# Performance work log

Hardware: AMD Instinct MI355X
Metric: run time of the kernel (lower is better)

## Reference

```python
import jax, jax.numpy as jnp
import numpy as np

B, C, H, W_IMG = 16, 3, 384, 384
P = 16
G = H // P                 # 24
NPATCH = G * G             # 576
SEQ = NPATCH + 1           # 577 (with cls token)
D, FF, NH, NL = 768, 3072, 12, 12
NCLS = 1000
K = int(0.5 * NPATCH)
HD = D // NH
EPS = 1e-6


def _ln(x, g, b):
    mu = jnp.mean(x, axis=-1, keepdims=True)
    var = jnp.mean((x - mu) ** 2, axis=-1, keepdims=True)
    return (x - mu) * jax.lax.rsqrt(var + EPS) * g + b


def setup_inputs() -> dict:
    key = jax.random.key(0)
    ks = jax.random.split(key, 12)
    s = 0.02
    return {
        "x": jax.random.normal(ks[0], (B, C, H, W_IMG), jnp.float32),
        "patch_w": jax.random.normal(ks[1], (D, C, P, P), jnp.float32) * s,
        "patch_b": jnp.zeros((D,), jnp.float32),
        "cls_tok": jax.random.normal(ks[2], (1, 1, D), jnp.float32) * s,
        "pos_emb": jax.random.normal(ks[3], (1, SEQ, D), jnp.float32) * s,
        "ln1_g": jnp.ones((NL, D), jnp.float32),
        "ln1_b": jnp.zeros((NL, D), jnp.float32),
        "Wqkv": jax.random.normal(ks[4], (NL, D, 3 * D), jnp.float32) * s,
        "bqkv": jnp.zeros((NL, 3 * D), jnp.float32),
        "Wo": jax.random.normal(ks[5], (NL, D, D), jnp.float32) * s,
        "bo": jnp.zeros((NL, D), jnp.float32),
        "ln2_g": jnp.ones((NL, D), jnp.float32),
        "ln2_b": jnp.zeros((NL, D), jnp.float32),
        "W1": jax.random.normal(ks[6], (NL, D, FF), jnp.float32) * s,
        "b1": jnp.zeros((NL, FF), jnp.float32),
        "W2": jax.random.normal(ks[7], (NL, FF, D), jnp.float32) * s,
        "b2": jnp.zeros((NL, D), jnp.float32),
        "lnf_g": jnp.ones((D,), jnp.float32),
        "lnf_b": jnp.zeros((D,), jnp.float32),
        "fc_w": jax.random.normal(ks[8], (D, NCLS), jnp.float32) * s,
        "fc_b": jnp.zeros((NCLS,), jnp.float32),
    }


def reference(x, patch_w, patch_b, cls_tok, pos_emb, ln1_g, ln1_b, Wqkv, bqkv,
              Wo, bo, ln2_g, ln2_b, W1, b1, W2, b2, lnf_g, lnf_b, fc_w, fc_b):
    b = x.shape[0]
    # patch embedding: strided conv -> (b, D, G, G) -> (b, NPATCH, D)
    patches = jax.lax.conv_general_dilated(
        x, patch_w, window_strides=(P, P), padding="VALID",
        dimension_numbers=("NCHW", "OIHW", "NCHW")) + patch_b[None, :, None, None]
    tok = patches.reshape(b, D, NPATCH).transpose(0, 2, 1)
    tok = jnp.concatenate([jnp.broadcast_to(cls_tok, (b, 1, D)), tok], axis=1)
    tok = tok + pos_emb  # seq matches original_seq_len, no resize

    # saliency = avg-pool of raw first input channel (net_G output is unused in the source)
    pooled = x[:, 0].reshape(b, G, P, G, P).mean(axis=(2, 4)).reshape(b, NPATCH)
    _, idx = jax.lax.top_k(jnp.abs(pooled), K)          # (b, K)
    spatial = tok[:, 1:, :]
    sel = jnp.take_along_axis(spatial, idx[:, :, None], axis=1)  # (b, K, D)
    h = jnp.concatenate([tok[:, :1, :], sel], axis=1)   # (b, K+1, D)
    S = h.shape[1]

    scale = 1.0 / np.sqrt(HD)
    for i in range(NL):
        y = _ln(h, ln1_g[i], ln1_b[i])
        qkv = y @ Wqkv[i] + bqkv[i]
        q, k_, v = jnp.split(qkv, 3, axis=-1)
        q = q.reshape(b, S, NH, HD)
        k_ = k_.reshape(b, S, NH, HD)
        v = v.reshape(b, S, NH, HD)
        att = jnp.einsum("bqhd,bkhd->bhqk", q, k_) * scale
        att = jax.nn.softmax(att, axis=-1)
        o = jnp.einsum("bhqk,bkhd->bqhd", att, v).reshape(b, S, D)
        h = h + (o @ Wo[i] + bo[i])
        y = _ln(h, ln2_g[i], ln2_b[i])
        h = h + (jax.nn.gelu(y @ W1[i] + b1[i], approximate=False) @ W2[i] + b2[i])

    cls_out = _ln(h, lnf_g, lnf_b)[:, 0]   # pool_type='tok'
    return cls_out @ fc_w + fc_b


if __name__ == "__main__":
    out = reference(**setup_inputs())
    print(out.shape)
```

## Files before the change

kernel.cpp:

```cpp
#include <hip/hip_runtime.h>
#include <hip/hip_bf16.h>
#include <math.h>

#define BB 16
#define SS 289
#define DD 768
#define FFD 3072
#define NHD 12
#define NLAY 12
#define KSEL 288
#define NPATCH 576

typedef short bf16x8 __attribute__((ext_vector_type(8)));
typedef short bf16x4 __attribute__((ext_vector_type(4)));
typedef float f32x4 __attribute__((ext_vector_type(4)));

typedef __attribute__((address_space(3))) void lds_t;
typedef __attribute__((address_space(1))) const void glb_t;

__device__ __forceinline__ void gload16(const void* g, void* l) {
    __builtin_amdgcn_global_load_lds((glb_t*)g, (lds_t*)l, 16, 0, 0);
}

__device__ __forceinline__ bf16x8 ds_read128(unsigned addr) {
    bf16x8 r;
    asm volatile("ds_read_b128 %0, %1" : "=v"(r) : "v"(addr));
    return r;
}

__device__ __forceinline__ float gelu_f(float v) {
    return 0.5f * v * (1.0f + erff(v * 0.70710678118654752f));
}

__device__ __forceinline__ void store_val(float* p, float v) { *p = v; }
__device__ __forceinline__ void store_val(__hip_bfloat16* p, float v) { *p = __float2bfloat16(v); }

__global__ __launch_bounds__(256) void pool_kernel(const float* __restrict__ x,
                                                   float* __restrict__ pooled) {
    int bp = blockIdx.x;
    int b = bp / NPATCH, p = bp - b * NPATCH;
    int gi = p / 24, gj = p - gi * 24;
    int tid = threadIdx.x;
    int pi = tid >> 4, pj = tid & 15;
    float v = x[((size_t)(b * 3) * 384 + gi * 16 + pi) * 384 + gj * 16 + pj];
    #pragma unroll
    for (int o = 32; o > 0; o >>= 1) v += __shfl_down(v, o);
    __shared__ float red[4];
    if ((tid & 63) == 0) red[tid >> 6] = v;
    __syncthreads();
    if (tid == 0) pooled[bp] = (red[0] + red[1] + red[2] + red[3]) * (1.0f / 256.0f);
}

__global__ __launch_bounds__(576) void topk_kernel(const float* __restrict__ pooled,
                                                   int* __restrict__ idxsel) {
    __shared__ float a[NPATCH];
    int b = blockIdx.x, tid = threadIdx.x;
    a[tid] = fabsf(pooled[b * NPATCH + tid]);
    __syncthreads();
    float mine = a[tid];
    int rank = 0;
    for (int j = 0; j < NPATCH; ++j) {
        float aj = a[j];
        rank += (aj > mine) || (aj == mine && j < tid);
    }
    if (rank < KSEL) idxsel[b * KSEL + rank] = tid;
}

__global__ __launch_bounds__(256) void convert_bf16(const float* __restrict__ in,
                                                    __hip_bfloat16* __restrict__ out,
                                                    int n) {
    int i = blockIdx.x * 256 + threadIdx.x;
    if (i < n) out[i] = __float2bfloat16(in[i]);
}

__global__ __launch_bounds__(256) void convert_layer(const float* __restrict__ wqkv,
                                                     const float* __restrict__ wo,
                                                     const float* __restrict__ w1,
                                                     const float* __restrict__ w2,
                                                     __hip_bfloat16* __restrict__ oqkv,
                                                     __hip_bfloat16* __restrict__ owo,
                                                     __hip_bfloat16* __restrict__ ow1,
                                                     __hip_bfloat16* __restrict__ ow2) {
    __shared__ float tb[32][33];
    int bid = blockIdx.x;
    const float* W; __hip_bfloat16* O; int K, N, tile;
    if (bid < 1728)      { W = wqkv; O = oqkv; K = 768;  N = 2304; tile = bid; }
    else if (bid < 2304) { W = wo;   O = owo;  K = 768;  N = 768;  tile = bid - 1728; }
    else if (bid < 4608) { W = w1;   O = ow1;  K = 768;  N = 3072; tile = bid - 2304; }
    else                 { W = w2;   O = ow2;  K = 3072; N = 768;  tile = bid - 4608; }
    int ntx = N >> 5;
    int n0 = (tile % ntx) << 5, k0 = (tile / ntx) << 5;
    int t = threadIdx.x;
    int r = t >> 3, c = (t & 7) << 2;
    float4 v = *(const float4*)&W[(size_t)(k0 + r) * N + n0 + c];
    tb[r][c] = v.x; tb[r][c + 1] = v.y; tb[r][c + 2] = v.z; tb[r][c + 3] = v.w;
    __syncthreads();
    int n = t >> 3, k = (t & 7) << 2;
    __hip_bfloat16* dst = &O[(size_t)(n0 + n) * K + k0 + k];
    #pragma unroll
    for (int j = 0; j < 4; ++j) dst[j] = __float2bfloat16(tb[k + j][n]);
}

__global__ __launch_bounds__(256) void im2col_kernel(const float* __restrict__ x,
                                                     const int* __restrict__ idxsel,
                                                     __hip_bfloat16* __restrict__ col) {
    int t = blockIdx.x;
    int b = t / KSEL, r = t - b * KSEL;
    int p = idxsel[b * KSEL + r];
    int gi = p / 24, gj = p - gi * 24;
    int tid = threadIdx.x;
    int pi = tid >> 4, pj = tid & 15;
    __hip_bfloat16* crow = col + (size_t)t * 768;
    #pragma unroll
    for (int c = 0; c < 3; ++c)
        crow[c * 256 + tid] = __float2bfloat16(
            x[((size_t)(b * 3 + c) * 384 + gi * 16 + pi) * 384 + gj * 16 + pj]);
}

__global__ __launch_bounds__(256) void assemble_tokens(const float* __restrict__ temp,
                                                       const float* __restrict__ cls_tok,
                                                       const float* __restrict__ pos_emb,
                                                       const int* __restrict__ idxsel,
                                                       float* __restrict__ h) {
    int row = blockIdx.x;
    int b = row / SS, s = row - b * SS;
    int tid = threadIdx.x;
    float* hrow = h + (size_t)row * DD;
    if (s == 0) {
        #pragma unroll
        for (int c = 0; c < 3; ++c) {
            int j = c * 256 + tid;
            hrow[j] = cls_tok[j] + pos_emb[j];
        }
    } else {
        int r = s - 1;
        int p = idxsel[b * KSEL + r];
        const float* trow = temp + (size_t)(b * KSEL + r) * DD;
        const float* pe = pos_emb + (size_t)(1 + p) * DD;
        #pragma unroll
        for (int c = 0; c < 3; ++c) {
            int j = c * 256 + tid;
            hrow[j] = trow[j] + pe[j];
        }
    }
}

template <typename T>
__global__ __launch_bounds__(256) void ln_kernel(const float* __restrict__ in,
                                                 T* __restrict__ out,
                                                 const float* __restrict__ g,
                                                 const float* __restrict__ be,
                                                 size_t in_stride) {
    int row = blockIdx.x;
    const float* r = in + (size_t)row * in_stride;
    T* w = out + (size_t)row * DD;
    int tid = threadIdx.x;
    float v0 = r[tid], v1 = r[256 + tid], v2 = r[512 + tid];
    float s = v0 + v1 + v2;
    #pragma unroll
    for (int o = 32; o > 0; o >>= 1) s += __shfl_down(s, o);
    __shared__ float red[4];
    if ((tid & 63) == 0) red[tid >> 6] = s;
    __syncthreads();
    float mu = (red[0] + red[1] + red[2] + red[3]) * (1.0f / 768.0f);
    float d0 = v0 - mu, d1 = v1 - mu, d2 = v2 - mu;
    float q = d0 * d0 + d1 * d1 + d2 * d2;
    #pragma unroll
    for (int o = 32; o > 0; o >>= 1) q += __shfl_down(q, o);
    __syncthreads();
    if ((tid & 63) == 0) red[tid >> 6] = q;
    __syncthreads();
    float var = (red[0] + red[1] + red[2] + red[3]) * (1.0f / 768.0f);
    float rs = rsqrtf(var + 1e-6f);
    store_val(&w[tid],       d0 * rs * g[tid]       + be[tid]);
    store_val(&w[256 + tid], d1 * rs * g[256 + tid] + be[256 + tid]);
    store_val(&w[512 + tid], d2 * rs * g[512 + tid] + be[512 + tid]);
}

template <typename OUT_T, int ACT, int RES, int SPLITK>
__global__ __launch_bounds__(512) void gemm_bf16(const __hip_bfloat16* __restrict__ A,
                                                 const __hip_bfloat16* __restrict__ BT,
                                                 OUT_T* __restrict__ C,
                                                 const float* __restrict__ bias,
                                                 const float* __restrict__ res,
                                                 float* __restrict__ part,
                                                 int M, int N, int K) {
    __shared__ __hip_bfloat16 smA[3][256 * 32];
    __shared__ __hip_bfloat16 smB[3][256 * 32];
    const int t = threadIdx.x;
    const int lane = t & 63, wid = t >> 6;
    const int wr = wid >> 2, wc = wid & 3;
    const int l15 = lane & 15, l4 = lane >> 4;

    const int gx = gridDim.x;
    const int nwg = gx * gridDim.y;
    const int orig = blockIdx.y * gx + blockIdx.x;
    const int q8 = nwg >> 3, r8 = nwg & 7;
    const int xcd = orig & 7, linb = orig >> 3;
    const int swz = (xcd < r8 ? xcd * (q8 + 1) : r8 * (q8 + 1) + (xcd - r8) * q8) + linb;
    const int m0 = (swz / gx) << 8;
    const int n0 = (swz - (swz / gx) * gx) << 8;

    const int Ksub = K / SPLITK;
    const int kz0 = blockIdx.z * Ksub;

    int ra[8], rb[4];
    #pragma unroll
    for (int f = 0; f < 8; ++f) {
        int ml = wr * 128 + f * 16 + l15;
        ra[f] = ml * 64 + ((l4 ^ ((ml >> 1) & 3)) << 4);
    }
    #pragma unroll
    for (int f = 0; f < 4; ++f) {
        int nl = wc * 64 + f * 16 + l15;
        rb[f] = nl * 64 + ((l4 ^ ((nl >> 1) & 3)) << 4);
    }

    size_t aoff[2], boff[2];
    #pragma unroll
    for (int it = 0; it < 2; ++it) {
        int s = it * 512 + t;
        int m = s >> 2;
        int kc = (s & 3) ^ ((m >> 1) & 3);
        int gm = m0 + m; if (gm > M - 1) gm = M - 1;
        aoff[it] = (size_t)gm * K + kz0 + kc * 8;
        boff[it] = (size_t)(n0 + m) * K + kz0 + kc * 8;
    }
    const int wb = wid << 10;
    const unsigned ldsA0 = (unsigned)(size_t)(lds_t*)&smA[0][0];
    const unsigned ldsB0 = (unsigned)(size_t)(lds_t*)&smB[0][0];

    auto STAGE = [&](int kt, int buf) {
        int k0e = kt << 5;
        gload16(A + aoff[0] + k0e,  (char*)(&smA[buf][0]) + wb);
        gload16(A + aoff[1] + k0e,  (char*)(&smA[buf][0]) + 8192 + wb);
        gload16(BT + boff[0] + k0e, (char*)(&smB[buf][0]) + wb);
        gload16(BT + boff[1] + k0e, (char*)(&smB[buf][0]) + 8192 + wb);
    };

    f32x4 acc[8][4];
    #pragma unroll
    for (int i = 0; i < 8; ++i)
        #pragma unroll
        for (int j = 0; j < 4; ++j) acc[i][j] = (f32x4){0.f, 0.f, 0.f, 0.f};

    const int nt = Ksub >> 5;
    STAGE(0, 0); STAGE(1, 1);
    int cur = 0, stb = 2;
    for (int kt = 0; kt < nt; ++kt) {
        if (kt + 1 < nt) asm volatile("s_waitcnt vmcnt(4)" ::: "memory");
        else             asm volatile("s_waitcnt vmcnt(0)" ::: "memory");
        asm volatile("s_barrier" ::: "memory");
        if (kt + 2 < nt) STAGE(kt + 2, stb);
        const unsigned sa = ldsA0 + cur * 16384u;
        const unsigned sb = ldsB0 + cur * 16384u;
        bf16x8 af[8], bf[4];
        #pragma unroll
        for (int f = 0; f < 8; ++f) af[f] = ds_read128(sa + ra[f]);
        #pragma unroll
        for (int f = 0; f < 4; ++f) bf[f] = ds_read128(sb + rb[f]);
        asm volatile("s_waitcnt lgkmcnt(0)" ::: "memory");
        __builtin_amdgcn_sched_barrier(0);
        #pragma unroll
        for (int i = 0; i < 8; ++i)
            #pragma unroll
            for (int j = 0; j < 4; ++j)
                acc[i][j] = __builtin_amdgcn_mfma_f32_16x16x32_bf16(af[i], bf[j], acc[i][j], 0, 0, 0);
        cur = cur == 2 ? 0 : cur + 1;
        stb = stb == 2 ? 0 : stb + 1;
    }

    if (SPLITK == 1) {
        #pragma unroll
        for (int i = 0; i < 8; ++i) {
            int gmb = m0 + wr * 128 + i * 16 + l4 * 4;
            #pragma unroll
            for (int j = 0; j < 4; ++j) {
                int gn = n0 + wc * 64 + j * 16 + l15;
                float bv = bias ? bias[gn] : 0.f;
                #pragma unroll
                for (int r = 0; r < 4; ++r) {
                    int gm = gmb + r;
                    if (gm < M) {
                        float v = acc[i][j][r] + bv;
                        if (ACT) v = gelu_f(v);
                        if (RES) v += res[(size_t)gm * N + gn];
                        store_val(&C[(size_t)gm * N + gn], v);
                    }
                }
            }
        }
    } else {
        float* pz = part + (size_t)blockIdx.z * M * N;
        #pragma unroll
        for (int i = 0; i < 8; ++i) {
            int gmb = m0 + wr * 128 + i * 16 + l4 * 4;
            #pragma unroll
            for (int j = 0; j < 4; ++j) {
                int gn = n0 + wc * 64 + j * 16 + l15;
                #pragma unroll
                for (int r = 0; r < 4; ++r) {
                    int gm = gmb + r;
                    if (gm < M) pz[(size_t)gm * N + gn] = acc[i][j][r];
                }
            }
        }
    }
}

template <int NPART>
__global__ __launch_bounds__(256) void combine_res(const float* __restrict__ part,
                                                   const float* __restrict__ bias,
                                                   float* __restrict__ h,
                                                   int MN, int N) {
    int i = (blockIdx.x * 256 + threadIdx.x) * 4;
    if (i >= MN) return;
    float4 v = *(const float4*)&part[i];
    #pragma unroll
    for (int z = 1; z < NPART; ++z) {
        float4 p = *(const float4*)&part[(size_t)z * MN + i];
        v.x += p.x; v.y += p.y; v.z += p.z; v.w += p.w;
    }
    int n = i % N;
    float4 bv = *(const float4*)&bias[n];
    float4 hv = *(const float4*)&h[i];
    v.x += bv.x + hv.x; v.y += bv.y + hv.y; v.z += bv.z + hv.z; v.w += bv.w + hv.w;
    *(float4*)&h[i] = v;
}

__global__ __launch_bounds__(256) void head_gemm(const float* __restrict__ yf,
                                                 const float* __restrict__ fc_w,
                                                 const float* __restrict__ fc_b,
                                                 float* __restrict__ out) {
    __shared__ float ylds[4 * 768];
    const int tid = threadIdx.x;
    const int mh = blockIdx.y * 4;
    for (int i = tid; i < 4 * 768; i += 256) ylds[i] = yf[(size_t)(mh + i / 768) * 768 + i % 768];
    __syncthreads();
    const int n = blockIdx.x * 256 + tid;
    if (n >= 1000) return;
    float acc0 = 0.f, acc1 = 0.f, acc2 = 0.f, acc3 = 0.f;
    for (int k = 0; k < 768; ++k) {
        float w = fc_w[(size_t)k * 1000 + n];
        acc0 = fmaf(ylds[k], w, acc0);
        acc1 = fmaf(ylds[768 + k], w, acc1);
        acc2 = fmaf(ylds[1536 + k], w, acc2);
        acc3 = fmaf(ylds[2304 + k], w, acc3);
    }
    float b = fc_b[n];
    out[(size_t)(mh + 0) * 1000 + n] = acc0 + b;
    out[(size_t)(mh + 1) * 1000 + n] = acc1 + b;
    out[(size_t)(mh + 2) * 1000 + n] = acc2 + b;
    out[(size_t)(mh + 3) * 1000 + n] = acc3 + b;
}

__global__ __launch_bounds__(64) void attn_fused(const __hip_bfloat16* __restrict__ qkv,
                                                 __hip_bfloat16* __restrict__ o) {
    __shared__ __hip_bfloat16 p_lds[32][40];
    __shared__ __hip_bfloat16 v_lds[32][68];
    const int qt = blockIdx.x, bh = blockIdx.y;
    const int b = bh / NHD, hd = bh - b * NHD;
    const int lane = threadIdx.x;
    const int l15 = lane & 15, l4 = lane >> 4;
    const size_t tb = (size_t)b * SS;
    const int hc = hd * 64;

    bf16x8 aq[2][2];
    #pragma unroll
    for (int qi = 0; qi < 2; ++qi) {
        int qr = qt * 32 + qi * 16 + l15;
        if (qr >= SS) qr = SS - 1;
        const __hip_bfloat16* qrow = qkv + (tb + qr) * 2304 + hc;
        #pragma unroll
        for (int kd = 0; kd < 2; ++kd)
            aq[qi][kd] = *(const bf16x8*)(qrow + kd * 32 + l4 * 8);
    }

    float m_run[2][4], l_run[2][4];
    f32x4 oa[2][4];
    #pragma unroll
    for (int qi = 0; qi < 2; ++qi)
        #pragma unroll
        for (int r = 0; r < 4; ++r) { m_run[qi][r] = -1e30f; l_run[qi][r] = 0.f; }
    #pragma unroll
    for (int qi = 0; qi < 2; ++qi)
        #pragma unroll
        for (int dt = 0; dt < 4; ++dt) oa[qi][dt] = (f32x4){0.f, 0.f, 0.f, 0.f};

    for (int kt = 0; kt < 10; ++kt) {
        const int kbase = kt * 32;
        bf16x4 vreg[8];
        #pragma unroll
        for (int it = 0; it < 8; ++it) {
            int vr = kbase + it * 4 + l4;
            if (vr >= SS) vr = SS - 1;
            vreg[it] = *(const bf16x4*)(qkv + (tb + vr) * 2304 + 1536 + hc + l15 * 4);
        }
        bf16x8 bk[2][2];
        #pragma unroll
        for (int ki = 0; ki < 2; ++ki) {
            int kr = kbase + ki * 16 + l15;
            if (kr >= SS) kr = SS - 1;
            const __hip_bfloat16* krow = qkv + (tb + kr) * 2304 + 768 + hc;
            #pragma unroll
            for (int kd = 0; kd < 2; ++kd)
                bk[ki][kd] = *(const bf16x8*)(krow + kd * 32 + l4 * 8);
        }
        f32x4 s[2][2];
        #pragma unroll
        for (int qi = 0; qi < 2; ++qi)
            #pragma unroll
            for (int ki = 0; ki < 2; ++ki) {
                f32x4 a = (f32x4){0.f, 0.f, 0.f, 0.f};
                #pragma unroll
                for (int kd = 0; kd < 2; ++kd)
                    a = __builtin_amdgcn_mfma_f32_16x16x32_bf16(aq[qi][kd], bk[ki][kd], a, 0, 0, 0);
                s[qi][ki] = a;
            }
        #pragma unroll
        for (int ki = 0; ki < 2; ++ki) {
            bool valid = (kbase + ki * 16 + l15) < SS;
            #pragma unroll
            for (int qi = 0; qi < 2; ++qi)
                #pragma unroll
                for (int r = 0; r < 4; ++r)
                    s[qi][ki][r] = valid ? s[qi][ki][r] * 0.125f : -1e30f;
        }
        float p[2][2][4];
        #pragma unroll
        for (int qi = 0; qi < 2; ++qi) {
            float tm[4];
            #pragma unroll
            for (int r = 0; r < 4; ++r) tm[r] = fmaxf(s[qi][0][r], s[qi][1][r]);
            #pragma unroll
            for (int sh = 1; sh < 16; sh <<= 1)
                #pragma unroll
                for (int r = 0; r < 4; ++r) tm[r] = fmaxf(tm[r], __shfl_xor(tm[r], sh));
            float rs[4];
            #pragma unroll
            for (int r = 0; r < 4; ++r) {
                float mn = fmaxf(m_run[qi][r], tm[r]);
                float corr = __expf(m_run[qi][r] - mn);
                m_run[qi][r] = mn;
                float p0 = __expf(s[qi][0][r] - mn);
                float p1 = __expf(s[qi][1][r] - mn);
                p[qi][0][r] = p0; p[qi][1][r] = p1;
                rs[r] = p0 + p1;
                l_run[qi][r] *= corr;
                #pragma unroll
                for (int dt = 0; dt < 4; ++dt) oa[qi][dt][r] *= corr;
            }
            #pragma unroll
            for (int sh = 1; sh < 16; sh <<= 1)
                #pragma unroll
                for (int r = 0; r < 4; ++r) rs[r] += __shfl_xor(rs[r], sh);
            #pragma unroll
            for (int r = 0; r < 4; ++r) l_run[qi][r] += rs[r];
        }
        #pragma unroll
        for (int qi = 0; qi < 2; ++qi)
            #pragma unroll
            for (int ki = 0; ki < 2; ++ki)
                #pragma unroll
                for (int r = 0; r < 4; ++r)
                    p_lds[qi * 16 + l4 * 4 + r][ki * 16 + l15] = __float2bfloat16(p[qi][ki][r]);
        #pragma unroll
        for (int it = 0; it < 8; ++it)
            *(bf16x4*)&v_lds[it * 4 + l4][l15 * 4] = vreg[it];
        __syncthreads();
        bf16x8 pa[2];
        #pragma unroll
        for (int qi = 0; qi < 2; ++qi)
            pa[qi] = *(const bf16x8*)&p_lds[qi * 16 + l15][l4 * 8];
        bf16x8 vb[4];
        #pragma unroll
        for (int dt = 0; dt < 4; ++dt) {
            bf16x8 v;
            #pragma unroll
            for (int j = 0; j < 8; ++j)
                v[j] = *(const short*)&v_lds[l4 * 8 + j][dt * 16 + l15];
            vb[dt] = v;
        }
        #pragma unroll
        for (int qi = 0; qi < 2; ++qi)
            #pragma unroll
            for (int dt = 0; dt < 4; ++dt)
                oa[qi][dt] = __builtin_amdgcn_mfma_f32_16x16x32_bf16(pa[qi], vb[dt], oa[qi][dt], 0, 0, 0);
        __syncthreads();
    }
    #pragma unroll
    for (int qi = 0; qi < 2; ++qi)
        #pragma unroll
        for (int r = 0; r < 4; ++r) {
            int q = qt * 32 + qi * 16 + l4 * 4 + r;
            if (q < SS) {
                float inv = 1.0f / l_run[qi][r];
                __hip_bfloat16* orow = o + (tb + q) * 768 + hc;
                #pragma unroll
                for (int dt = 0; dt < 4; ++dt)
                    orow[dt * 16 + l15] = __float2bfloat16(oa[qi][dt][r] * inv);
            }
        }
}

static const size_t OFF_POOLED = 0;
static const size_t OFF_IDX    = 10240;
static const size_t OFF_H      = 16384;
static const size_t OFF_YB     = 3567616;
static const size_t OFF_OB     = 5343232;
static const size_t OFF_QKVB   = 7118848;
static const size_t OFF_WBUF   = 12445696;
static const size_t OFF_PWB    = 15984640;
static const size_t OFF_YF     = 16279552;
static const size_t OFF_BIG    = 16291840;
static const size_t OFF_PART   = 23394304;

extern "C" void kernel_launch(void* const* d_in, const int* in_sizes, int n_in,
                              void* d_out, int out_size, void* d_ws, size_t ws_size,
                              hipStream_t stream) {
    const float* x       = (const float*)d_in[0];
    const float* patch_w = (const float*)d_in[1];
    const float* patch_b = (const float*)d_in[2];
    const float* cls_tok = (const float*)d_in[3];
    const float* pos_emb = (const float*)d_in[4];
    const float* ln1_g   = (const float*)d_in[5];
    const float* ln1_b   = (const float*)d_in[6];
    const float* Wqkv    = (const float*)d_in[7];
    const float* bqkv    = (const float*)d_in[8];
    const float* Wo      = (const float*)d_in[9];
    const float* bo      = (const float*)d_in[10];
    const float* ln2_g   = (const float*)d_in[11];
    const float* ln2_b   = (const float*)d_in[12];
    const float* W1      = (const float*)d_in[13];
    const float* b1      = (const float*)d_in[14];
    const float* W2      = (const float*)d_in[15];
    const float* b2      = (const float*)d_in[16];
    const float* lnf_g   = (const float*)d_in[17];
    const float* lnf_b   = (const float*)d_in[18];
    const float* fc_w    = (const float*)d_in[19];
    const float* fc_b    = (const float*)d_in[20];
    float* out = (float*)d_out;
    float* ws  = (float*)d_ws;

    float*          pooled = ws + OFF_POOLED;
    int*            idxsel = (int*)(ws + OFF_IDX);
    float*          h      = ws + OFF_H;
    __hip_bfloat16* yb     = (__hip_bfloat16*)(ws + OFF_YB);
    __hip_bfloat16* ob     = (__hip_bfloat16*)(ws + OFF_OB);
    __hip_bfloat16* qkvb   = (__hip_bfloat16*)(ws + OFF_QKVB);
    __hip_bfloat16* wbuf   = (__hip_bfloat16*)(ws + OFF_WBUF);
    __hip_bfloat16* pwb    = (__hip_bfloat16*)(ws + OFF_PWB);
    float*          yf     = ws + OFF_YF;
    float*          big    = ws + OFF_BIG;
    float*          part   = ws + OFF_PART;
    __hip_bfloat16* col    = (__hip_bfloat16*)big;
    float*          temp   = big + 1769472;
    __hip_bfloat16* hidden = (__hip_bfloat16*)big;

    __hip_bfloat16* wqkvT = wbuf;
    __hip_bfloat16* woT   = wbuf + 1769472;
    __hip_bfloat16* w1T   = wbuf + 2359296;
    __hip_bfloat16* w2T   = wbuf + 4718592;

    const int M = BB * SS;
    const int MG2 = 19;
    const int MN = M * DD;

    pool_kernel<<<BB * NPATCH, 256, 0, stream>>>(x, pooled);
    topk_kernel<<<BB, 576, 0, stream>>>(pooled, idxsel);
    convert_bf16<<<(589824 + 255) / 256, 256, 0, stream>>>(patch_w, pwb, 589824);
    im2col_kernel<<<BB * KSEL, 256, 0, stream>>>(x, idxsel, col);
    gemm_bf16<float, 0, 0, 1><<<dim3(3, 18), 512, 0, stream>>>(
        col, pwb, temp, patch_b, nullptr, nullptr, 4608, DD, DD);
    assemble_tokens<<<BB * SS, 256, 0, stream>>>(temp, cls_tok, pos_emb, idxsel, h);

    for (int i = 0; i < NLAY; ++i) {
        convert_layer<<<6912, 256, 0, stream>>>(Wqkv + (size_t)i * DD * 3 * DD,
                                                Wo + (size_t)i * DD * DD,
                                                W1 + (size_t)i * DD * FFD,
                                                W2 + (size_t)i * FFD * DD,
                                                wqkvT, woT, w1T, w2T);

        ln_kernel<__hip_bfloat16><<<M, 256, 0, stream>>>(h, yb, ln1_g + i * DD, ln1_b + i * DD, DD);
        gemm_bf16<__hip_bfloat16, 0, 0, 1><<<dim3(9, MG2), 512, 0, stream>>>(
            yb, wqkvT, qkvb, bqkv + (size_t)i * 3 * DD, nullptr, nullptr, M, 3 * DD, DD);
        attn_fused<<<dim3(10, BB * NHD), 64, 0, stream>>>(qkvb, ob);
        gemm_bf16<float, 0, 0, 2><<<dim3(3, MG2, 2), 512, 0, stream>>>(
            ob, woT, (float*)nullptr, nullptr, nullptr, part, M, DD, DD);
        combine_res<2><<<(MN / 4 + 255) / 256, 256, 0, stream>>>(part, bo + (size_t)i * DD, h, MN, DD);
        ln_kernel<__hip_bfloat16><<<M, 256, 0, stream>>>(h, yb, ln2_g + i * DD, ln2_b + i * DD, DD);
        gemm_bf16<__hip_bfloat16, 1, 0, 1><<<dim3(12, MG2), 512, 0, stream>>>(
            yb, w1T, hidden, b1 + (size_t)i * FFD, nullptr, nullptr, M, FFD, DD);
        gemm_bf16<float, 0, 0, 4><<<dim3(3, MG2, 4), 512, 0, stream>>>(
            hidden, w2T, (float*)nullptr, nullptr, nullptr, part, M, DD, FFD);
        combine_res<4><<<(MN / 4 + 255) / 256, 256, 0, stream>>>(part, b2 + (size_t)i * DD, h, MN, DD);
    }

    ln_kernel<float><<<BB, 256, 0, stream>>>(h, yf, lnf_g, lnf_b, (size_t)SS * DD);
    head_gemm<<<dim3(4, 4), 256, 0, stream>>>(yf, fc_w, fc_b, out);
}
```

Measured before the change: 2.799 ms.

## Shrink GEMM tile to 256x128 with 4 waves and split-K the classifier head

The bf16 GEMM tile drops from 256x256 with 8 waves to 256x128 with 4 waves. Each wave still computes a 128x64 sub-tile, and the LDS B buffer is halved, so more workgroups launch per GEMM and fill more CUs. The cost is lower A-tile reuse, because A is loaded twice as often for the same N. The classifier head is also reworked to one row per block with a two-way K split reduced through LDS, giving many more blocks than the old 16.

```diff
diff --git a/kernel.cpp b/kernel.cpp
--- a/kernel.cpp
+++ b/kernel.cpp
@@ -178,7 +178,7 @@
 }
 
 template <typename OUT_T, int ACT, int RES, int SPLITK>
-__global__ __launch_bounds__(512) void gemm_bf16(const __hip_bfloat16* __restrict__ A,
+__global__ __launch_bounds__(256) void gemm_bf16(const __hip_bfloat16* __restrict__ A,
                                                  const __hip_bfloat16* __restrict__ BT,
                                                  OUT_T* __restrict__ C,
                                                  const float* __restrict__ bias,
@@ -186,10 +186,10 @@
                                                  float* __restrict__ part,
                                                  int M, int N, int K) {
     __shared__ __hip_bfloat16 smA[3][256 * 32];
-    __shared__ __hip_bfloat16 smB[3][256 * 32];
+    __shared__ __hip_bfloat16 smB[3][128 * 32];
     const int t = threadIdx.x;
     const int lane = t & 63, wid = t >> 6;
-    const int wr = wid >> 2, wc = wid & 3;
+    const int wr = wid >> 1, wc = wid & 1;
     const int l15 = lane & 15, l4 = lane >> 4;
 
     const int gx = gridDim.x;
@@ -199,7 +199,7 @@
     const int xcd = orig & 7, linb = orig >> 3;
     const int swz = (xcd < r8 ? xcd * (q8 + 1) : r8 * (q8 + 1) + (xcd - r8) * q8) + linb;
     const int m0 = (swz / gx) << 8;
-    const int n0 = (swz - (swz / gx) * gx) << 8;
+    const int n0 = (swz - (swz / gx) * gx) << 7;
 
     const int Ksub = K / SPLITK;
     const int kz0 = blockIdx.z * Ksub;
@@ -216,14 +216,20 @@
         rb[f] = nl * 64 + ((l4 ^ ((nl >> 1) & 3)) << 4);
     }
 
-    size_t aoff[2], boff[2];
-    #pragma unroll
-    for (int it = 0; it < 2; ++it) {
-        int s = it * 512 + t;
+    size_t aoff[4], boff[2];
+    #pragma unroll
+    for (int it = 0; it < 4; ++it) {
+        int s = it * 256 + t;
         int m = s >> 2;
         int kc = (s & 3) ^ ((m >> 1) & 3);
         int gm = m0 + m; if (gm > M - 1) gm = M - 1;
         aoff[it] = (size_t)gm * K + kz0 + kc * 8;
+    }
+    #pragma unroll
+    for (int it = 0; it < 2; ++it) {
+        int s = it * 256 + t;
+        int m = s >> 2;
+        int kc = (s & 3) ^ ((m >> 1) & 3);
         boff[it] = (size_t)(n0 + m) * K + kz0 + kc * 8;
     }
     const int wb = wid << 10;
@@ -232,10 +238,12 @@
 
     auto STAGE = [&](int kt, int buf) {
         int k0e = kt << 5;
-        gload16(A + aoff[0] + k0e,  (char*)(&smA[buf][0]) + wb);
-        gload16(A + aoff[1] + k0e,  (char*)(&smA[buf][0]) + 8192 + wb);
-        gload16(BT + boff[0] + k0e, (char*)(&smB[buf][0]) + wb);
-        gload16(BT + boff[1] + k0e, (char*)(&smB[buf][0]) + 8192 + wb);
+        #pragma unroll
+        for (int it = 0; it < 4; ++it)
+            gload16(A + aoff[it] + k0e, (char*)(&smA[buf][0]) + it * 4096 + wb);
+        #pragma unroll
+        for (int it = 0; it < 2; ++it)
+            gload16(BT + boff[it] + k0e, (char*)(&smB[buf][0]) + it * 4096 + wb);
     };
 
     f32x4 acc[8][4];
@@ -248,12 +256,12 @@
     STAGE(0, 0); STAGE(1, 1);
     int cur = 0, stb = 2;
     for (int kt = 0; kt < nt; ++kt) {
-        if (kt + 1 < nt) asm volatile("s_waitcnt vmcnt(4)" ::: "memory");
+        if (kt + 1 < nt) asm volatile("s_waitcnt vmcnt(6)" ::: "memory");
         else             asm volatile("s_waitcnt vmcnt(0)" ::: "memory");
         asm volatile("s_barrier" ::: "memory");
         if (kt + 2 < nt) STAGE(kt + 2, stb);
         const unsigned sa = ldsA0 + cur * 16384u;
-        const unsigned sb = ldsB0 + cur * 16384u;
+        const unsigned sb = ldsB0 + cur * 8192u;
         bf16x8 af[8], bf[4];
         #pragma unroll
         for (int f = 0; f < 8; ++f) af[f] = ds_read128(sa + ra[f]);
@@ -332,26 +340,23 @@
                                                  const float* __restrict__ fc_w,
                                                  const float* __restrict__ fc_b,
                                                  float* __restrict__ out) {
-    __shared__ float ylds[4 * 768];
+    __shared__ float part[128];
     const int tid = threadIdx.x;
-    const int mh = blockIdx.y * 4;
-    for (int i = tid; i < 4 * 768; i += 256) ylds[i] = yf[(size_t)(mh + i / 768) * 768 + i % 768];
+    const int nl = tid & 127, kh = tid >> 7;
+    const int m = blockIdx.y;
+    const int n = blockIdx.x * 128 + nl;
+    float acc = 0.f;
+    if (n < 1000) {
+        const float* yr = yf + (size_t)m * 768 + kh * 384;
+        const float* wp = fc_w + (size_t)kh * 384 * 1000 + n;
+        #pragma unroll 4
+        for (int k = 0; k < 384; ++k)
+            acc = fmaf(yr[k], wp[(size_t)k * 1000], acc);
+    }
+    if (kh == 1) part[nl] = acc;
     __syncthreads();
-    const int n = blockIdx.x * 256 + tid;
-    if (n >= 1000) return;
-    float acc0 = 0.f, acc1 = 0.f, acc2 = 0.f, acc3 = 0.f;
-    for (int k = 0; k < 768; ++k) {
-        float w = fc_w[(size_t)k * 1000 + n];
-        acc0 = fmaf(ylds[k], w, acc0);
-        acc1 = fmaf(ylds[768 + k], w, acc1);
-        acc2 = fmaf(ylds[1536 + k], w, acc2);
-        acc3 = fmaf(ylds[2304 + k], w, acc3);
-    }
-    float b = fc_b[n];
-    out[(size_t)(mh + 0) * 1000 + n] = acc0 + b;
-    out[(size_t)(mh + 1) * 1000 + n] = acc1 + b;
-    out[(size_t)(mh + 2) * 1000 + n] = acc2 + b;
-    out[(size_t)(mh + 3) * 1000 + n] = acc3 + b;
+    if (kh == 0 && n < 1000)
+        out[(size_t)m * 1000 + n] = acc + part[nl] + fc_b[n];
 }
 
 __global__ __launch_bounds__(64) void attn_fused(const __hip_bfloat16* __restrict__ qkv,
@@ -563,14 +568,14 @@
     __hip_bfloat16* w2T   = wbuf + 4718592;
 
     const int M = BB * SS;
-    const int MG2 = 19;
+    const int MG = 19;
     const int MN = M * DD;
 
     pool_kernel<<<BB * NPATCH, 256, 0, stream>>>(x, pooled);
     topk_kernel<<<BB, 576, 0, stream>>>(pooled, idxsel);
     convert_bf16<<<(589824 + 255) / 256, 256, 0, stream>>>(patch_w, pwb, 589824);
     im2col_kernel<<<BB * KSEL, 256, 0, stream>>>(x, idxsel, col);
-    gemm_bf16<float, 0, 0, 1><<<dim3(3, 18), 512, 0, stream>>>(
+    gemm_bf16<float, 0, 0, 1><<<dim3(6, 18), 256, 0, stream>>>(
         col, pwb, temp, patch_b, nullptr, nullptr, 4608, DD, DD);
     assemble_tokens<<<BB * SS, 256, 0, stream>>>(temp, cls_tok, pos_emb, idxsel, h);
 
@@ -582,20 +587,20 @@
                                                 wqkvT, woT, w1T, w2T);
 
         ln_kernel<__hip_bfloat16><<<M, 256, 0, stream>>>(h, yb, ln1_g + i * DD, ln1_b + i * DD, DD);
-        gemm_bf16<__hip_bfloat16, 0, 0, 1><<<dim3(9, MG2), 512, 0, stream>>>(
+        gemm_bf16<__hip_bfloat16, 0, 0, 1><<<dim3(18, MG), 256, 0, stream>>>(
             yb, wqkvT, qkvb, bqkv + (size_t)i * 3 * DD, nullptr, nullptr, M, 3 * DD, DD);
         attn_fused<<<dim3(10, BB * NHD), 64, 0, stream>>>(qkvb, ob);
-        gemm_bf16<float, 0, 0, 2><<<dim3(3, MG2, 2), 512, 0, stream>>>(
+        gemm_bf16<float, 0, 0, 2><<<dim3(6, MG, 2), 256, 0, stream>>>(
             ob, woT, (float*)nullptr, nullptr, nullptr, part, M, DD, DD);
         combine_res<2><<<(MN / 4 + 255) / 256, 256, 0, stream>>>(part, bo + (size_t)i * DD, h, MN, DD);
         ln_kernel<__hip_bfloat16><<<M, 256, 0, stream>>>(h, yb, ln2_g + i * DD, ln2_b + i * DD, DD);
-        gemm_bf16<__hip_bfloat16, 1, 0, 1><<<dim3(12, MG2), 512, 0, stream>>>(
+        gemm_bf16<__hip_bfloat16, 1, 0, 1><<<dim3(24, MG), 256, 0, stream>>>(
             yb, w1T, hidden, b1 + (size_t)i * FFD, nullptr, nullptr, M, FFD, DD);
-        gemm_bf16<float, 0, 0, 4><<<dim3(3, MG2, 4), 512, 0, stream>>>(
+        gemm_bf16<float, 0, 0, 4><<<dim3(6, MG, 4), 256, 0, stream>>>(
             hidden, w2T, (float*)nullptr, nullptr, nullptr, part, M, DD, FFD);
         combine_res<4><<<(MN / 4 + 255) / 256, 256, 0, stream>>>(part, b2 + (size_t)i * DD, h, MN, DD);
     }
 
     ln_kernel<float><<<BB, 256, 0, stream>>>(h, yf, lnf_g, lnf_b, (size_t)SS * DD);
-    head_gemm<<<dim3(4, 4), 256, 0, stream>>>(yf, fc_w, fc_b, out);
-}
+    head_gemm<<<dim3(8, 16), 256, 0, stream>>>(yf, fc_w, fc_b, out);
+}
```

Result: slower. 3.433 ms (+22.7%).
